# Optimization experiments

Hardware: AMD Instinct MI355X
Metric: run time of the kernel (lower is better)

The kernel has to match this reference:

```python
import jax, jax.numpy as jnp
import numpy as np

N, E, G = 50000, 400000, 64
DIN, HID, H, ED = 128, 32, 8, 5
HC = H * HID            # 256, conv3 out_channels (concat=False, heads=1)
LH, DOUT = 256, 32
NEG_SLOPE = 0.2


def setup_inputs() -> dict:
    key = jax.random.key(0)
    ks = jax.random.split(key, 32)
    rn = lambda k, s, sc=0.05: (jax.random.normal(k, s, jnp.float32) * sc)
    inp = {
        "x": jax.random.normal(ks[0], (N, DIN), jnp.float32),
        "edge_index": jax.random.randint(ks[1], (2, E), 0, N, jnp.int32),
        "edge_attr": jax.random.uniform(ks[2], (E, ED), jnp.float32),
        "batch": jnp.sort(jax.random.randint(ks[3], (N,), 0, G, jnp.int32)),
        # conv1: in=DIN, heads=H, out=HID, concat=True
        "W1": rn(ks[4], (DIN, H * HID)), "as1": rn(ks[5], (H, HID)), "ad1": rn(ks[6], (H, HID)),
        "We1": rn(ks[7], (ED, H * HID)), "ae1": rn(ks[8], (H, HID)), "b1": jnp.zeros((H * HID,), jnp.float32),
        # conv2: in=H*HID, heads=H, out=HID, concat=True
        "W2": rn(ks[9], (H * HID, H * HID)), "as2": rn(ks[10], (H, HID)), "ad2": rn(ks[11], (H, HID)),
        "We2": rn(ks[12], (ED, H * HID)), "ae2": rn(ks[13], (H, HID)), "b2": jnp.zeros((H * HID,), jnp.float32),
        # conv3: in=H*HID, heads=1, out=HC, concat=False
        "W3": rn(ks[14], (H * HID, HC)), "as3": rn(ks[15], (1, HC)), "ad3": rn(ks[16], (1, HC)),
        "We3": rn(ks[17], (ED, HC)), "ae3": rn(ks[18], (1, HC)), "b3": jnp.zeros((HC,), jnp.float32),
        # MLP head
        "fcW1": rn(ks[19], (HC, LH)), "fcb1": jnp.zeros((LH,), jnp.float32),
        "fcW2": rn(ks[20], (LH, DOUT)), "fcb2": jnp.zeros((DOUT,), jnp.float32),
    }
    return inp


def gat_layer(x, src, dst, ea, W, att_s, att_d, We, att_e, bias, heads, out_ch, concat):
    n = x.shape[0]
    h = (x @ W).reshape(n, heads, out_ch)                 # [N,H,C]
    e = (ea @ We).reshape(-1, heads, out_ch)              # [E,H,C]
    a_s = (h * att_s).sum(-1)                             # [N,H]
    a_d = (h * att_d).sum(-1)                             # [N,H]
    a_e = (e * att_e).sum(-1)                             # [E,H]
    alpha = jax.nn.leaky_relu(a_s[src] + a_d[dst] + a_e, NEG_SLOPE)  # [E,H]
    m = jax.ops.segment_max(alpha, dst, num_segments=n)   # segment softmax over dst
    p = jnp.exp(alpha - m[dst])
    denom = jax.ops.segment_sum(p, dst, num_segments=n)
    w = p / (denom[dst] + 1e-16)                          # [E,H]
    msg = h[src] * w[:, :, None]                          # [E,H,C]
    out = jax.ops.segment_sum(msg, dst, num_segments=n)   # [N,H,C]
    out = out.reshape(n, heads * out_ch) if concat else out.mean(axis=1)
    return out + bias


def reference(x, edge_index, edge_attr, batch,
              W1, as1, ad1, We1, ae1, b1,
              W2, as2, ad2, We2, ae2, b2,
              W3, as3, ad3, We3, ae3, b3,
              fcW1, fcb1, fcW2, fcb2):
    src, dst = edge_index[0], edge_index[1]
    h = jax.nn.elu(gat_layer(x, src, dst, edge_attr, W1, as1, ad1, We1, ae1, b1, H, HID, True))
    h = jax.nn.elu(gat_layer(h, src, dst, edge_attr, W2, as2, ad2, We2, ae2, b2, H, HID, True))
    h = jax.nn.elu(gat_layer(h, src, dst, edge_attr, W3, as3, ad3, We3, ae3, b3, 1, HC, False))
    h = jax.nn.gelu(h @ fcW1 + fcb1, approximate=False) @ fcW2 + fcb2   # [N,DOUT]
    # global_mean_pool over batch ids
    sums = jax.ops.segment_sum(h, batch, num_segments=G)
    cnt = jax.ops.segment_sum(jnp.ones((h.shape[0],), h.dtype), batch, num_segments=G)
    return sums / jnp.maximum(cnt, 1.0)[:, None]
```

## Files before the change

### kernel.cpp

```cpp
#include <hip/hip_runtime.h>
#include <math.h>


#define N_NODES 50000
#define N_EDGES 400000
#define N_GRAPH 64
#define DIN     128
#define NHC     256
#define DOUT    32

typedef _Float16 f16x8 __attribute__((ext_vector_type(8)));
typedef _Float16 f16x4 __attribute__((ext_vector_type(4)));
typedef float    f32x4 __attribute__((ext_vector_type(4)));

#define LDP2 72

__global__ __launch_bounds__(256) void mfma_gemm_kernel(
    const _Float16* __restrict__ Ah, const _Float16* __restrict__ Bh,
    const float* __restrict__ bias, _Float16* __restrict__ Ch,
    const float* __restrict__ asl, const float* __restrict__ adl,
    float* __restrict__ asb, float* __restrict__ adb,
    const int* __restrict__ batch, float* __restrict__ pooled,
    int nrow, int K, int mode)
{
    __shared__ __align__(16) _Float16 sAh[128][LDP2];
    __shared__ __align__(16) _Float16 sBh[64][LDP2];

    const int tid = threadIdx.x, lane = tid & 63, wid = tid >> 6;
    const int wm = wid & 1, wn = wid >> 1;

    int xt, yt;
    if (gridDim.x == 4) {
        int bid = blockIdx.x + (blockIdx.y << 2);
        yt = (bid >> 5) * 8 + (bid & 7);
        xt = (bid >> 3) & 3;
    } else { xt = blockIdx.x; yt = blockIdx.y; }
    const int row0 = yt * 128, col0 = xt * 64;
    if (row0 >= nrow) return;

    const int frow = lane & 15, fk = (lane >> 4) * 8;
    const int rs = tid >> 3, cs = (tid & 7) * 8;

    f32x4 acc[4][2] = {};
    f16x8 pA[4], pB[2];

#pragma unroll
    for (int p = 0; p < 4; p++) {
        int idx = tid + p * 256;
        int r = idx >> 3, ch = (idx & 7) * 8;
        int gr = row0 + r;
        pA[p] = (gr < nrow) ? *(const f16x8*)(Ah + (long)gr * K + ch) : (f16x8)0;
    }
#pragma unroll
    for (int p = 0; p < 2; p++) {
        int idx = tid + p * 256;
        int r = idx >> 3, ch = (idx & 7) * 8;
        pB[p] = *(const f16x8*)(Bh + (long)(col0 + r) * K + ch);
    }

    for (int k0 = 0; k0 < K; k0 += 64) {
#pragma unroll
        for (int p = 0; p < 4; p++) {
            int idx = tid + p * 256;
            *(f16x8*)&sAh[idx >> 3][(idx & 7) * 8] = pA[p];
        }
#pragma unroll
        for (int p = 0; p < 2; p++) {
            int idx = tid + p * 256;
            *(f16x8*)&sBh[idx >> 3][(idx & 7) * 8] = pB[p];
        }
        __syncthreads();

        if (k0 + 64 < K) {
            int kn = k0 + 64;
#pragma unroll
            for (int p = 0; p < 4; p++) {
                int idx = tid + p * 256;
                int r = idx >> 3, ch = (idx & 7) * 8;
                int gr = row0 + r;
                pA[p] = (gr < nrow) ? *(const f16x8*)(Ah + (long)gr * K + kn + ch) : (f16x8)0;
            }
#pragma unroll
            for (int p = 0; p < 2; p++) {
                int idx = tid + p * 256;
                int r = idx >> 3, ch = (idx & 7) * 8;
                pB[p] = *(const f16x8*)(Bh + (long)(col0 + r) * K + kn + ch);
            }
        }

#pragma unroll
        for (int sub = 0; sub < 2; sub++) {
            const int fks = fk + sub * 32;
            f16x8 bh[2];
#pragma unroll
            for (int nt = 0; nt < 2; nt++)
                bh[nt] = *(const f16x8*)&sBh[wn * 32 + nt * 16 + frow][fks];
#pragma unroll
            for (int mt = 0; mt < 4; mt++) {
                f16x8 ah = *(const f16x8*)&sAh[wm * 64 + mt * 16 + frow][fks];
#pragma unroll
                for (int nt = 0; nt < 2; nt++)
                    acc[mt][nt] = __builtin_amdgcn_mfma_f32_16x16x32_f16(ah, bh[nt], acc[mt][nt], 0, 0, 0);
            }
        }
        __syncthreads();
    }

    const int crow0 = row0 + wm * 64 + (lane >> 4) * 4;
    const int ccol0 = col0 + wn * 32 + (lane & 15);

    if (mode == 0) {
#pragma unroll
        for (int mt = 0; mt < 4; mt++)
#pragma unroll
            for (int nt = 0; nt < 2; nt++) {
                int col = ccol0 + nt * 16;
#pragma unroll
                for (int r = 0; r < 4; r++) {
                    int row = crow0 + mt * 16 + r;
                    if (row < nrow) Ch[(long)row * 256 + col] = (_Float16)acc[mt][nt][r];
                }
            }
        if (asl != nullptr) {
            const float asl0 = asl[ccol0], asl1 = asl[ccol0 + 16];
            const float adl0 = adl[ccol0], adl1 = adl[ccol0 + 16];
            const int headw = (col0 + wn * 32) >> 5;
#pragma unroll
            for (int mt = 0; mt < 4; mt++) {
#pragma unroll
                for (int r = 0; r < 4; r++) {
                    float s = acc[mt][0][r] * asl0 + acc[mt][1][r] * asl1;
                    float d = acc[mt][0][r] * adl0 + acc[mt][1][r] * adl1;
                    s += __shfl_xor(s, 1); s += __shfl_xor(s, 2);
                    s += __shfl_xor(s, 4); s += __shfl_xor(s, 8);
                    d += __shfl_xor(d, 1); d += __shfl_xor(d, 2);
                    d += __shfl_xor(d, 4); d += __shfl_xor(d, 8);
                    if ((lane & 15) == 0) {
                        int row = crow0 + mt * 16 + r;
                        if (row < nrow) {
                            asb[row * 8 + headw] = s;
                            adb[row * 8 + headw] = d;
                        }
                    }
                }
            }
        }
    } else {
        float* pool = (float*)&sAh[0][0];
        const int g0 = batch[row0];
        const int rlast = (row0 + 127 < nrow) ? row0 + 127 : nrow - 1;
        const int gspan = batch[rlast] - g0 + 1;
        const bool fits = (gspan <= 16);
        for (int i = tid; i < 16 * 64; i += 256) pool[i] = 0.f;
        __syncthreads();

        const float b0 = bias[ccol0], b1 = bias[ccol0 + 16];
        const int lc0 = ccol0 - col0, lc1 = lc0 + 16;
        float sum0 = 0.f, sum1 = 0.f;
        int curg = -1;
#pragma unroll
        for (int mt = 0; mt < 4; mt++) {
#pragma unroll
            for (int r = 0; r < 4; r++) {
                int row = crow0 + mt * 16 + r;
                if (row >= nrow) continue;
                int g = batch[row];
                if (g != curg) {
                    if (curg >= 0) {
                        if (fits) {
                            atomicAdd(&pool[(curg - g0) * 64 + lc0], sum0);
                            atomicAdd(&pool[(curg - g0) * 64 + lc1], sum1);
                        } else {
                            atomicAdd(&pooled[curg * 256 + ccol0], sum0);
                            atomicAdd(&pooled[curg * 256 + ccol0 + 16], sum1);
                        }
                    }
                    curg = g; sum0 = 0.f; sum1 = 0.f;
                }
                float v0 = acc[mt][0][r] + b0;
                float v1 = acc[mt][1][r] + b1;
                sum0 += 0.5f * v0 * (1.f + erff(v0 * 0.7071067811865475f));
                sum1 += 0.5f * v1 * (1.f + erff(v1 * 0.7071067811865475f));
            }
        }
        if (curg >= 0) {
            if (fits) {
                atomicAdd(&pool[(curg - g0) * 64 + lc0], sum0);
                atomicAdd(&pool[(curg - g0) * 64 + lc1], sum1);
            } else {
                atomicAdd(&pooled[curg * 256 + ccol0], sum0);
                atomicAdd(&pooled[curg * 256 + ccol0 + 16], sum1);
            }
        }
        __syncthreads();
        if (fits) {
            for (int i = tid; i < gspan * 64; i += 256) {
                float val = pool[i];
                if (val != 0.f)
                    atomicAdd(&pooled[(g0 + (i >> 6)) * 256 + col0 + (i & 63)], val);
            }
        }
    }
}

#define J0 1600000
#define J1 32768
#define J2 65536
#define J3 65536
#define J4 65536
#define J5 16384
#define J6 N_NODES
#define J7 64
#define JTOT (J0+J1+J2+J3+J4+J5+J6+J7)

__device__ __forceinline__ void t_one(const float* W, _Float16* Bh,
                                      int id, int K, int realN)
{
    int n = id / K, k = id - n * K;
    Bh[id] = (_Float16)W[(long)k * realN + n];
}

__global__ __launch_bounds__(256) void prep_kernel(
    const float* __restrict__ x,
    const float* __restrict__ W1, const float* __restrict__ W2, const float* __restrict__ W3,
    const float* __restrict__ F1,
    _Float16* __restrict__ xh,
    _Float16* __restrict__ W1th, _Float16* __restrict__ W2th,
    _Float16* __restrict__ W3th, _Float16* __restrict__ F1th,
    float* __restrict__ pooled, int* __restrict__ deg, int* __restrict__ gcnt)
{
    int idx = blockIdx.x * 256 + threadIdx.x;
    if (idx < J0) {
        float4 v = ((const float4*)x)[idx];
        f16x4 h;
        h[0] = (_Float16)v.x; h[1] = (_Float16)v.y;
        h[2] = (_Float16)v.z; h[3] = (_Float16)v.w;
        *(f16x4*)(xh + (long)idx * 4) = h;
        return;
    }
    idx -= J0;
    if (idx < J1) { t_one(W1, W1th, idx, DIN, NHC); return; }
    idx -= J1;
    if (idx < J2) { t_one(W2, W2th, idx, NHC, NHC); return; }
    idx -= J2;
    if (idx < J3) { t_one(W3, W3th, idx, NHC, NHC); return; }
    idx -= J3;
    if (idx < J4) { t_one(F1, F1th, idx, NHC, NHC); return; }
    idx -= J4;
    if (idx < J5) { pooled[idx] = 0.f; return; }
    idx -= J5;
    if (idx < J6) { deg[idx] = 0; return; }
    idx -= J6;
    if (idx < J7) { gcnt[idx] = 0; return; }
}

__global__ void me_all_kernel(
    const float* __restrict__ We1, const float* __restrict__ ae1,
    const float* __restrict__ We2, const float* __restrict__ ae2,
    const float* __restrict__ We3, const float* __restrict__ ae3,
    float* __restrict__ MeAll)
{
    int l = blockIdx.x;
    const float* We = (l == 0) ? We1 : (l == 1) ? We2 : We3;
    const float* ae = (l == 0) ? ae1 : (l == 1) ? ae2 : ae3;
    int H = (l == 2) ? 1 : 8, C = (l == 2) ? 256 : 32;
    int t = threadIdx.x;
    if (t >= 5 * H) return;
    int j = t / H, hh = t - j * H;
    float s = 0.f;
    for (int c = 0; c < C; c++) s += We[j * NHC + hh * C + c] * ae[hh * C + c];
    MeAll[l * 40 + j * H + hh] = s;
}

__global__ __launch_bounds__(256) void asd_kernel(
    const _Float16* __restrict__ h, const float* __restrict__ atts, const float* __restrict__ attd,
    float* __restrict__ asb, float* __restrict__ adb, int total)
{
    int n = blockIdx.x * 256 + threadIdx.x;
    if (n >= total) return;
    const f16x8* hp = (const f16x8*)(h + (long)n * NHC);
    const float4* sp = (const float4*)atts;
    const float4* dp = (const float4*)attd;
    float ss = 0.f, dd = 0.f;
    for (int c = 0; c < NHC / 8; c++) {
        f16x8 hv = hp[c];
        float4 s1 = sp[2 * c], s2 = sp[2 * c + 1];
        float4 d1 = dp[2 * c], d2 = dp[2 * c + 1];
        ss += (float)hv[0] * s1.x + (float)hv[1] * s1.y + (float)hv[2] * s1.z + (float)hv[3] * s1.w
            + (float)hv[4] * s2.x + (float)hv[5] * s2.y + (float)hv[6] * s2.z + (float)hv[7] * s2.w;
        dd += (float)hv[0] * d1.x + (float)hv[1] * d1.y + (float)hv[2] * d1.z + (float)hv[3] * d1.w
            + (float)hv[4] * d2.x + (float)hv[5] * d2.y + (float)hv[6] * d2.z + (float)hv[7] * d2.w;
    }
    asb[n * 8] = ss; adb[n * 8] = dd;
}

__global__ __launch_bounds__(256) void count_hist_kernel(
    const int* __restrict__ ei, const int* __restrict__ batch,
    int* __restrict__ deg, int* __restrict__ gcnt, int E, int N)
{
    __shared__ int hist[N_GRAPH];
    int t = threadIdx.x;
    if (t < N_GRAPH) hist[t] = 0;
    __syncthreads();
    int i = blockIdx.x * 256 + t;
    if (i < E) atomicAdd(&deg[ei[E + i]], 1);
    if (i < N) atomicAdd(&hist[batch[i]], 1);
    __syncthreads();
    if (t < N_GRAPH && hist[t] > 0) atomicAdd(&gcnt[t], hist[t]);
}

__global__ __launch_bounds__(256) void scan_block_kernel(
    const int* __restrict__ deg, int* __restrict__ rowstart, int* __restrict__ partial, int n)
{
    __shared__ int s[256];
    int i = blockIdx.x * 256 + threadIdx.x;
    int v = (i < n) ? deg[i] : 0;
    s[threadIdx.x] = v;
    __syncthreads();
    for (int off = 1; off < 256; off <<= 1) {
        int t = (threadIdx.x >= off) ? s[threadIdx.x - off] : 0;
        __syncthreads();
        s[threadIdx.x] += t;
        __syncthreads();
    }
    if (i < n) rowstart[i] = s[threadIdx.x] - v;
    if (threadIdx.x == 255) partial[blockIdx.x] = s[255];
}

__global__ __launch_bounds__(256) void scan_partial_kernel(int* __restrict__ partial, int nb)
{
    __shared__ int s[256];
    int v = (threadIdx.x < nb) ? partial[threadIdx.x] : 0;
    s[threadIdx.x] = v;
    __syncthreads();
    for (int off = 1; off < 256; off <<= 1) {
        int t = (threadIdx.x >= off) ? s[threadIdx.x - off] : 0;
        __syncthreads();
        s[threadIdx.x] += t;
        __syncthreads();
    }
    if (threadIdx.x < nb) partial[threadIdx.x] = s[threadIdx.x] - v;
}

__global__ __launch_bounds__(256) void scan_add_kernel(
    int* __restrict__ rowstart, const int* __restrict__ partial, int* __restrict__ cursor,
    int n, int E)
{
    int i = blockIdx.x * 256 + threadIdx.x;
    if (i < n) {
        int v = rowstart[i] + partial[blockIdx.x];
        rowstart[i] = v;
        cursor[i] = v;
    }
    if (i == 0) rowstart[n] = E;
}

__global__ __launch_bounds__(256) void fill_kernel(
    const int* __restrict__ ei, int* __restrict__ cursor, int2* __restrict__ csr, int E)
{
    int e = blockIdx.x * 256 + threadIdx.x;
    if (e >= E) return;
    int dst = ei[E + e];
    int pos = atomicAdd(&cursor[dst], 1);
    csr[pos] = make_int2(ei[e], e);
}

__global__ __launch_bounds__(256) void gat_agg_kernel(
    const int* __restrict__ rowstart, const int2* __restrict__ csr,
    const float* __restrict__ ea, const float* __restrict__ asb,
    const float* __restrict__ adb, const float* __restrict__ MeL,
    const _Float16* __restrict__ h, const float* __restrict__ bias,
    _Float16* __restrict__ Oh, int H, int clog2)
{
    int node = blockIdx.x * 4 + (threadIdx.x >> 6);
    if (node >= N_NODES) return;
    int lane = threadIdx.x & 63;
    int c0 = lane * 4;
    int hc = c0 >> clog2;
    int heff = lane & (H - 1);
    float Mh0 = MeL[0 * H + heff], Mh1 = MeL[1 * H + heff], Mh2 = MeL[2 * H + heff],
          Mh3 = MeL[3 * H + heff], Mh4 = MeL[4 * H + heff];
    float adn = adb[node * 8 + heff];
    int beg = rowstart[node], end = rowstart[node + 1];
    float ax = 0.f, ay = 0.f, az = 0.f, aw = 0.f, den = 0.f;
    for (int i = beg; i < end; i += 8) {
        int idx = i + (lane >> 3);
        if (idx >= end) idx = end - 1;
        int2 se = csr[idx];
        const float* eap = ea + (long)se.y * 5;
        float aeh = eap[0] * Mh0 + eap[1] * Mh1 + eap[2] * Mh2 + eap[3] * Mh3 + eap[4] * Mh4;
        float al = asb[se.x * 8 + heff] + adn + aeh;
        al = fmaxf(al, 0.2f * al);
        float pv = expf(al);
        int nrem = end - i;
#pragma unroll
        for (int j = 0; j < 8; j++) {
            if (j >= nrem) break;
            float pj  = __shfl(pv, j * 8 + hc);
            int  srcj = __shfl(se.x, j * 8);
            const f16x4 hv = *(const f16x4*)(h + (long)srcj * NHC + c0);
            den += pj;
            ax += pj * (float)hv[0]; ay += pj * (float)hv[1];
            az += pj * (float)hv[2]; aw += pj * (float)hv[3];
        }
    }
    float w = 1.0f / (den + 1e-16f);
    const float4 bv = *(const float4*)(bias + c0);
    float4 v;
    v.x = ax * w + bv.x;  v.y = ay * w + bv.y;
    v.z = az * w + bv.z;  v.w = aw * w + bv.w;
    v.x = (v.x > 0.f) ? v.x : expm1f(v.x);
    v.y = (v.y > 0.f) ? v.y : expm1f(v.y);
    v.z = (v.z > 0.f) ? v.z : expm1f(v.z);
    v.w = (v.w > 0.f) ? v.w : expm1f(v.w);
    f16x4 oh;
    oh[0] = (_Float16)v.x; oh[1] = (_Float16)v.y;
    oh[2] = (_Float16)v.z; oh[3] = (_Float16)v.w;
    *(f16x4*)(Oh + (long)node * NHC + c0) = oh;
}

__global__ void final_kernel(const float* __restrict__ pooled, const int* __restrict__ gcnt,
                             const float* __restrict__ fcW2, const float* __restrict__ fcb2,
                             float* __restrict__ out)
{
    int g = blockIdx.x;
    int j = threadIdx.x;
    if (j >= DOUT) return;
    float s = 0.f;
    for (int k = 0; k < NHC; k++) s += pooled[g * NHC + k] * fcW2[k * DOUT + j];
    int c = gcnt[g];
    out[g * DOUT + j] = (c > 0) ? (s / (float)c + fcb2[j]) : 0.f;
}

extern "C" void kernel_launch(void* const* d_in, const int* in_sizes, int n_in,
                              void* d_out, int out_size, void* d_ws, size_t ws_size,
                              hipStream_t stream)
{
    const float* x    = (const float*)d_in[0];
    const int*   ei   = (const int*)  d_in[1];
    const float* ea   = (const float*)d_in[2];
    const int*   bat  = (const int*)  d_in[3];
    const float* W[3]   = {(const float*)d_in[4],  (const float*)d_in[10], (const float*)d_in[16]};
    const float* Asl[3] = {(const float*)d_in[5],  (const float*)d_in[11], (const float*)d_in[17]};
    const float* Adl[3] = {(const float*)d_in[6],  (const float*)d_in[12], (const float*)d_in[18]};
    const float* Wel[3] = {(const float*)d_in[7],  (const float*)d_in[13], (const float*)d_in[19]};
    const float* Ael[3] = {(const float*)d_in[8],  (const float*)d_in[14], (const float*)d_in[20]};
    const float* Bil[3] = {(const float*)d_in[9],  (const float*)d_in[15], (const float*)d_in[21]};
    const float* fcW1 = (const float*)d_in[22];
    const float* fcb1 = (const float*)d_in[23];
    const float* fcW2 = (const float*)d_in[24];
    const float* fcb2 = (const float*)d_in[25];

    char* w = (char*)d_ws;
    _Float16* h    = (_Float16*)w;     w += (size_t)N_NODES * NHC * 2;
    _Float16* xh   = (_Float16*)w;     w += (size_t)N_NODES * DIN * 2;
    _Float16* xbh  = (_Float16*)w;     w += (size_t)N_NODES * NHC * 2;
    float*    asb  = (float*)w;        w += (size_t)N_NODES * 8 * 4;
    float*    adb  = (float*)w;        w += (size_t)N_NODES * 8 * 4;
    float*    MeAll= (float*)w;        w += 120 * 4;
    float*    pooled=(float*)w;        w += (size_t)N_GRAPH * NHC * 4;
    _Float16* W1th = (_Float16*)w;     w += (size_t)NHC * DIN * 2;
    _Float16* W2th = (_Float16*)w;     w += (size_t)NHC * NHC * 2;
    _Float16* W3th = (_Float16*)w;     w += (size_t)NHC * NHC * 2;
    _Float16* F1th = (_Float16*)w;     w += (size_t)NHC * NHC * 2;
    int* gcnt     = (int*)w;           w += N_GRAPH * 4;
    int* deg      = (int*)w;           w += (size_t)N_NODES * 4;
    int* rowstart = (int*)w;           w += (size_t)(N_NODES + 1) * 4;
    int* cursor   = (int*)w;           w += (size_t)N_NODES * 4;
    int* partial  = (int*)w;           w += 256 * 4;
    w = (char*)(((size_t)w + 15) & ~(size_t)15);
    int2* csr     = (int2*)w;          w += (size_t)N_EDGES * 8;

    const int NB = (N_NODES + 255) / 256;

    prep_kernel<<<(JTOT + 255) / 256, 256, 0, stream>>>(
        x, W[0], W[1], W[2], fcW1,
        xh, W1th, W2th, W3th, F1th,
        pooled, deg, gcnt);
    count_hist_kernel<<<(N_EDGES + 255) / 256, 256, 0, stream>>>(ei, bat, deg, gcnt, N_EDGES, N_NODES);
    scan_block_kernel<<<NB, 256, 0, stream>>>(deg, rowstart, partial, N_NODES);
    scan_partial_kernel<<<1, 256, 0, stream>>>(partial, NB);
    scan_add_kernel<<<NB, 256, 0, stream>>>(rowstart, partial, cursor, N_NODES, N_EDGES);
    fill_kernel<<<(N_EDGES + 255) / 256, 256, 0, stream>>>(ei, cursor, csr, N_EDGES);
    me_all_kernel<<<3, 64, 0, stream>>>(Wel[0], Ael[0], Wel[1], Ael[1], Wel[2], Ael[2], MeAll);

    const int Hs[3] = {8, 8, 1};
    const int CL[3] = {5, 5, 8};
    const int Ks[3] = {DIN, NHC, NHC};

    const dim3 ggrid(4, 392);

    const _Float16* curh = xh;
    const _Float16* Wth[3] = {W1th, W2th, W3th};
    for (int l = 0; l < 3; l++) {
        const int H = Hs[l];
        const bool fuse = (l != 2);
        mfma_gemm_kernel<<<ggrid, 256, 0, stream>>>(
            curh, Wth[l], nullptr, h,
            fuse ? Asl[l] : nullptr, fuse ? Adl[l] : nullptr, asb, adb,
            nullptr, nullptr,
            N_NODES, Ks[l], 0);
        if (!fuse)
            asd_kernel<<<(N_NODES + 255) / 256, 256, 0, stream>>>(
                h, Asl[l], Adl[l], asb, adb, N_NODES);
        gat_agg_kernel<<<(N_NODES + 3) / 4, 256, 0, stream>>>(
            rowstart, csr, ea, asb, adb, MeAll + l * 40, h, Bil[l], xbh, H, CL[l]);
        curh = xbh;
    }

    mfma_gemm_kernel<<<ggrid, 256, 0, stream>>>(
        xbh, F1th, fcb1, nullptr,
        nullptr, nullptr, nullptr, nullptr,
        bat, pooled,
        N_NODES, NHC, 3);
    final_kernel<<<N_GRAPH, 64, 0, stream>>>(pooled, gcnt, fcW2, fcb2, (float*)d_out);
}
```

Baseline: 447.6 us.

## Precompute per-edge attention terms in CSR order and widen aggregation loads

The fill kernel now computes the edge-attention contribution for all three layers once, storing it as fp16 in CSR order, so the aggregation kernel reads a contiguous per-edge value instead of gathering five edge_attr floats through a stored edge id. The CSR entries shrink to the source index only. Aggregation is restructured so each half-wave handles alternating edges with 8-wide fp16 loads, followed by a cross-half shuffle reduction. This costs extra workspace and writes in fill, and rounds the edge term to fp16.

```diff
diff --git a/kernel.cpp b/kernel.cpp
--- a/kernel.cpp
+++ b/kernel.cpp
@@ -39,7 +39,6 @@
     if (row0 >= nrow) return;
 
     const int frow = lane & 15, fk = (lane >> 4) * 8;
-    const int rs = tid >> 3, cs = (tid & 7) * 8;
 
     f32x4 acc[4][2] = {};
     f16x8 pA[4], pB[2];
@@ -356,67 +355,100 @@
 }
 
 __global__ __launch_bounds__(256) void fill_kernel(
-    const int* __restrict__ ei, int* __restrict__ cursor, int2* __restrict__ csr, int E)
+    const int* __restrict__ ei, const float* __restrict__ ea,
+    const float* __restrict__ MeAll, int* __restrict__ cursor,
+    int* __restrict__ csr, _Float16* __restrict__ aec, int E)
 {
     int e = blockIdx.x * 256 + threadIdx.x;
     if (e >= E) return;
     int dst = ei[E + e];
     int pos = atomicAdd(&cursor[dst], 1);
-    csr[pos] = make_int2(ei[e], e);
+    csr[pos] = ei[e];
+    const float* eap = ea + (long)e * 5;
+    float e0 = eap[0], e1 = eap[1], e2 = eap[2], e3 = eap[3], e4 = eap[4];
+#pragma unroll
+    for (int l = 0; l < 2; l++) {
+        const float* Me = MeAll + l * 40;
+        f16x8 v;
+#pragma unroll
+        for (int hh = 0; hh < 8; hh++) {
+            float s = e0 * Me[hh] + e1 * Me[8 + hh] + e2 * Me[16 + hh]
+                    + e3 * Me[24 + hh] + e4 * Me[32 + hh];
+            v[hh] = (_Float16)s;
+        }
+        *(f16x8*)(aec + (long)l * N_EDGES * 8 + (long)pos * 8) = v;
+    }
+    const float* Me2 = MeAll + 80;
+    float s2 = e0 * Me2[0] + e1 * Me2[1] + e2 * Me2[2] + e3 * Me2[3] + e4 * Me2[4];
+    f16x8 v2;
+#pragma unroll
+    for (int hh = 0; hh < 8; hh++) v2[hh] = (_Float16)s2;
+    *(f16x8*)(aec + (long)2 * N_EDGES * 8 + (long)pos * 8) = v2;
 }
 
 __global__ __launch_bounds__(256) void gat_agg_kernel(
-    const int* __restrict__ rowstart, const int2* __restrict__ csr,
-    const float* __restrict__ ea, const float* __restrict__ asb,
-    const float* __restrict__ adb, const float* __restrict__ MeL,
+    const int* __restrict__ rowstart, const int* __restrict__ csr,
+    const _Float16* __restrict__ aec, const float* __restrict__ asb,
+    const float* __restrict__ adb,
     const _Float16* __restrict__ h, const float* __restrict__ bias,
     _Float16* __restrict__ Oh, int H, int clog2)
 {
     int node = blockIdx.x * 4 + (threadIdx.x >> 6);
     if (node >= N_NODES) return;
-    int lane = threadIdx.x & 63;
-    int c0 = lane * 4;
-    int hc = c0 >> clog2;
-    int heff = lane & (H - 1);
-    float Mh0 = MeL[0 * H + heff], Mh1 = MeL[1 * H + heff], Mh2 = MeL[2 * H + heff],
-          Mh3 = MeL[3 * H + heff], Mh4 = MeL[4 * H + heff];
-    float adn = adb[node * 8 + heff];
-    int beg = rowstart[node], end = rowstart[node + 1];
-    float ax = 0.f, ay = 0.f, az = 0.f, aw = 0.f, den = 0.f;
+    const int lane = threadIdx.x & 63;
+    const int half = lane >> 5;
+    const int c8   = (lane & 31) * 8;
+    const int hc   = c8 >> clog2;
+    const int heff = lane & (H - 1);
+    const int grp  = lane >> 3;
+
+    const float adn = adb[node * 8 + heff];
+    const int beg = rowstart[node], end = rowstart[node + 1];
+
+    float acc[8] = {};
+    float den = 0.f;
+
     for (int i = beg; i < end; i += 8) {
-        int idx = i + (lane >> 3);
-        if (idx >= end) idx = end - 1;
-        int2 se = csr[idx];
-        const float* eap = ea + (long)se.y * 5;
-        float aeh = eap[0] * Mh0 + eap[1] * Mh1 + eap[2] * Mh2 + eap[3] * Mh3 + eap[4] * Mh4;
-        float al = asb[se.x * 8 + heff] + adn + aeh;
+        int idx = i + grp;
+        const bool valid = (idx < end);
+        if (!valid) idx = end - 1;
+        const int sj = csr[idx];
+        const float ae = (float)aec[(long)idx * 8 + heff];
+        float al = asb[sj * 8 + heff] + adn + ae;
         al = fmaxf(al, 0.2f * al);
-        float pv = expf(al);
-        int nrem = end - i;
-#pragma unroll
-        for (int j = 0; j < 8; j++) {
-            if (j >= nrem) break;
-            float pj  = __shfl(pv, j * 8 + hc);
-            int  srcj = __shfl(se.x, j * 8);
-            const f16x4 hv = *(const f16x4*)(h + (long)srcj * NHC + c0);
+        const float pv = valid ? expf(al) : 0.f;
+#pragma unroll
+        for (int jj = 0; jj < 4; jj++) {
+            const int j = jj * 2 + half;
+            const float pj = __shfl(pv, j * 8 + hc);
+            const int srcj = __shfl(sj, j * 8);
+            const f16x8 hv = *(const f16x8*)(h + (long)srcj * NHC + c8);
             den += pj;
-            ax += pj * (float)hv[0]; ay += pj * (float)hv[1];
-            az += pj * (float)hv[2]; aw += pj * (float)hv[3];
-        }
-    }
-    float w = 1.0f / (den + 1e-16f);
-    const float4 bv = *(const float4*)(bias + c0);
-    float4 v;
-    v.x = ax * w + bv.x;  v.y = ay * w + bv.y;
-    v.z = az * w + bv.z;  v.w = aw * w + bv.w;
-    v.x = (v.x > 0.f) ? v.x : expm1f(v.x);
-    v.y = (v.y > 0.f) ? v.y : expm1f(v.y);
-    v.z = (v.z > 0.f) ? v.z : expm1f(v.z);
-    v.w = (v.w > 0.f) ? v.w : expm1f(v.w);
-    f16x4 oh;
-    oh[0] = (_Float16)v.x; oh[1] = (_Float16)v.y;
-    oh[2] = (_Float16)v.z; oh[3] = (_Float16)v.w;
-    *(f16x4*)(Oh + (long)node * NHC + c0) = oh;
+#pragma unroll
+            for (int k = 0; k < 8; k++)
+                acc[k] += pj * (float)hv[k];
+        }
+    }
+
+    den += __shfl_xor(den, 32);
+#pragma unroll
+    for (int k = 0; k < 8; k++)
+        acc[k] += __shfl_xor(acc[k], 32);
+
+    if (half == 0) {
+        const float w = 1.0f / (den + 1e-16f);
+        const float4 b0 = *(const float4*)(bias + c8);
+        const float4 b1 = *(const float4*)(bias + c8 + 4);
+        const float bb[8] = {b0.x, b0.y, b0.z, b0.w, b1.x, b1.y, b1.z, b1.w};
+        f16x8 oh;
+#pragma unroll
+        for (int k = 0; k < 8; k++) {
+            float v = acc[k] * w + bb[k];
+            v = (v > 0.f) ? v : expm1f(v);
+            oh[k] = (_Float16)v;
+        }
+        *(f16x8*)(Oh + (long)node * NHC + c8) = oh;
+    }
 }
 
 __global__ void final_kernel(const float* __restrict__ pooled, const int* __restrict__ gcnt,
@@ -469,7 +501,9 @@
     int* cursor   = (int*)w;           w += (size_t)N_NODES * 4;
     int* partial  = (int*)w;           w += 256 * 4;
     w = (char*)(((size_t)w + 15) & ~(size_t)15);
-    int2* csr     = (int2*)w;          w += (size_t)N_EDGES * 8;
+    int* csr      = (int*)w;           w += (size_t)N_EDGES * 4;
+    w = (char*)(((size_t)w + 15) & ~(size_t)15);
+    _Float16* aec = (_Float16*)w;      w += (size_t)3 * N_EDGES * 8 * 2;
 
     const int NB = (N_NODES + 255) / 256;
 
@@ -481,8 +515,8 @@
     scan_block_kernel<<<NB, 256, 0, stream>>>(deg, rowstart, partial, N_NODES);
     scan_partial_kernel<<<1, 256, 0, stream>>>(partial, NB);
     scan_add_kernel<<<NB, 256, 0, stream>>>(rowstart, partial, cursor, N_NODES, N_EDGES);
-    fill_kernel<<<(N_EDGES + 255) / 256, 256, 0, stream>>>(ei, cursor, csr, N_EDGES);
     me_all_kernel<<<3, 64, 0, stream>>>(Wel[0], Ael[0], Wel[1], Ael[1], Wel[2], Ael[2], MeAll);
+    fill_kernel<<<(N_EDGES + 255) / 256, 256, 0, stream>>>(ei, ea, MeAll, cursor, csr, aec, N_EDGES);
 
     const int Hs[3] = {8, 8, 1};
     const int CL[3] = {5, 5, 8};
@@ -504,7 +538,7 @@
             asd_kernel<<<(N_NODES + 255) / 256, 256, 0, stream>>>(
                 h, Asl[l], Adl[l], asb, adb, N_NODES);
         gat_agg_kernel<<<(N_NODES + 3) / 4, 256, 0, stream>>>(
-            rowstart, csr, ea, asb, adb, MeAll + l * 40, h, Bil[l], xbh, H, CL[l]);
+            rowstart, csr, aec + (size_t)l * N_EDGES * 8, asb, adb, h, Bil[l], xbh, H, CL[l]);
         curh = xbh;
     }
 
```

Result: faster. 431.9 us (-3.5%).
